# Optimization experiments

Measured on AMD Instinct MI355X. Metric: run time of the kernel, lower is better.

The kernel has to match this reference:

```python
import math
import jax, jax.numpy as jnp
import numpy as np

B, S, D, H, DFF, BASE = 2, 2048, 1024, 16, 4096, 10000.0
HD = D // H  # 64


def setup_inputs() -> dict:
    key = jax.random.key(0)
    ks = jax.random.split(key, 16)
    sc = 0.02
    inp = {
        "x": jax.random.normal(ks[0], (B, S, D), jnp.float32),
        "positions": jnp.arange(S, dtype=jnp.int32),
        "wq": jax.random.normal(ks[1], (D, D), jnp.float32) * sc,
        "bq": jnp.zeros((D,), jnp.float32),
        "wk": jax.random.normal(ks[2], (D, D), jnp.float32) * sc,
        "bk": jnp.zeros((D,), jnp.float32),
        "wv": jax.random.normal(ks[3], (D, D), jnp.float32) * sc,
        "bv": jnp.zeros((D,), jnp.float32),
        "wo": jax.random.normal(ks[4], (D, D), jnp.float32) * sc,
        "bo": jnp.zeros((D,), jnp.float32),
        "phase_bias": jax.random.uniform(ks[5], (H, HD), jnp.float32, -2.0 * math.pi, 0.0),
        "w1": jax.random.normal(ks[6], (D, DFF), jnp.float32) * sc,
        "b1": jnp.zeros((DFF,), jnp.float32),
        "w2": jax.random.normal(ks[7], (DFF, D), jnp.float32) * sc,
        "b2": jnp.zeros((D,), jnp.float32),
        "g1": jnp.ones((D,), jnp.float32),
        "be1": jnp.zeros((D,), jnp.float32),
        "g2": jnp.ones((D,), jnp.float32),
        "be2": jnp.zeros((D,), jnp.float32),
    }
    return inp


def _layernorm(x, g, b):
    mu = jnp.mean(x, -1, keepdims=True)
    var = jnp.mean(jnp.square(x - mu), -1, keepdims=True)
    return (x - mu) / jnp.sqrt(var + 1e-5) * g + b


def _block(x, positions, wq, bq, wk, bk, wv, bv, wo, bo, phase_bias,
           w1, b1, w2, b2, g1, be1, g2, be2):
    # projections -> (B, H, S, HD)
    def heads(w, b):
        return (x @ w + b).reshape(B, S, H, HD).transpose(0, 2, 1, 3)
    q, k, v = heads(wq, bq), heads(wk, bk), heads(wv, bv)

    # PoPE: magnitudes via softplus, phases from position*freq (+ clamped bias for k)
    mu_q = jax.nn.softplus(q)
    mu_k = jax.nn.softplus(k)
    freqs = 1.0 / BASE ** (jnp.arange(HD, dtype=jnp.float32) / HD)      # (HD,)
    pos_ph = positions[:, None].astype(jnp.float32) * freqs[None, :]     # (S, HD)
    q_ph = pos_ph[None, None]                                            # (1,1,S,HD)
    cb = jnp.clip(phase_bias, -2.0 * math.pi, 0.0)
    k_ph = pos_ph[None, None] + cb[None, :, None, :]                     # (1,H,S,HD)
    q_p = jnp.concatenate([mu_q * jnp.cos(q_ph), mu_q * jnp.sin(q_ph)], -1)  # (B,H,S,2HD)
    k_p = jnp.concatenate([mu_k * jnp.cos(k_ph), mu_k * jnp.sin(k_ph)], -1)

    # manual attention with causal mask and softmax1
    scale = 1.0 / math.sqrt(2 * HD)
    scores = jnp.einsum("bhqd,bhkd->bhqk", q_p, k_p) * scale
    causal = jnp.triu(jnp.ones((S, S), bool), 1)
    scores = jnp.where(causal, -jnp.inf, scores)
    m = jnp.max(scores, -1, keepdims=True)  # finite: diagonal always unmasked
    e = jnp.exp(scores - m)
    w = e / (jnp.exp(-m) + jnp.sum(e, -1, keepdims=True))
    attn = jnp.einsum("bhqk,bhkd->bhqd", w, v)
    attn = attn.transpose(0, 2, 1, 3).reshape(B, S, D) @ wo + bo

    h = _layernorm(x + attn, g1, be1)
    ff = jax.nn.relu(h @ w1 + b1) @ w2 + b2
    return _layernorm(h + ff, g2, be2)


def reference(x, positions, wq, bq, wk, bk, wv, bv, wo, bo, phase_bias,
              w1, b1, w2, b2, g1, be1, g2, be2):
    return _block(x, positions, wq, bq, wk, bk, wv, bv, wo, bo, phase_bias,
                  w1, b1, w2, b2, g1, be1, g2, be2)
```

## Files before the change

### kernel.cpp

```cpp
#include <hip/hip_runtime.h>
#include <hip/hip_bf16.h>
#include <math.h>

#define NB 2
#define NS 2048
#define ND 1024
#define NH 16
#define NHD 64
#define NDFF 4096

typedef __attribute__((ext_vector_type(4))) float f32x4;
typedef __attribute__((ext_vector_type(8))) short bf16x8;

__device__ __forceinline__ short f2bf(float f) {
  union { float f; unsigned u; } v; v.f = f;
  unsigned r = v.u + 0x7fffu + ((v.u >> 16) & 1u);
  return (short)(r >> 16);
}
__device__ __forceinline__ float bf2f(unsigned short u) {
  union { unsigned u; float f; } v; v.u = ((unsigned)u) << 16; return v.f;
}
__device__ __forceinline__ float softplus_f(float x) {
  return fmaxf(x, 0.f) + log1pf(__expf(-fabsf(x)));
}
__device__ __forceinline__ void gl16(const short* g, short* l) {
  __builtin_amdgcn_global_load_lds(
      (const __attribute__((address_space(1))) void*)g,
      (__attribute__((address_space(3))) void*)l, 16, 0, 0);
}
__device__ __forceinline__ void xcd_map(int& row0, int& col0) {
  const int gx = gridDim.x, gy = gridDim.y;
  const int bid = blockIdx.y * gx + blockIdx.x;
  const int rows_px = gy >> 3;
  const int xcd = bid & 7, l = bid >> 3;
  row0 = (xcd * rows_px + (l % rows_px)) * 128;
  col0 = (l / rows_px) * 128;
}

__global__ __launch_bounds__(256) void k_wt6(
    const float* __restrict__ wq, const float* __restrict__ wk,
    const float* __restrict__ wv, const float* __restrict__ wo,
    const float* __restrict__ w1, const float* __restrict__ w2,
    short* __restrict__ wqT, short* __restrict__ wkT, short* __restrict__ wvT,
    short* __restrict__ woT, short* __restrict__ w1T, short* __restrict__ w2T) {
  __shared__ float t[64][65];
  const int bid = blockIdx.x;
  const float* W; short* Wt; int K, N, local;
  if (bid < 1024) {
    const int wsel = bid >> 8; local = bid & 255;
    W  = wsel == 0 ? wq  : wsel == 1 ? wk  : wsel == 2 ? wv  : wo;
    Wt = wsel == 0 ? wqT : wsel == 1 ? wkT : wsel == 2 ? wvT : woT;
    K = ND; N = ND;
  } else if (bid < 2048) {
    local = bid - 1024; W = w1; Wt = w1T; K = ND; N = NDFF;
  } else {
    local = bid - 2048; W = w2; Wt = w2T; K = NDFF; N = ND;
  }
  const int nx = N >> 6;
  const int n0 = (local % nx) * 64, k0 = (local / nx) * 64;
  for (int i = threadIdx.x; i < 4096; i += 256) {
    const int r = i >> 6, c = i & 63;
    t[r][c] = W[(size_t)(k0 + r) * N + n0 + c];
  }
  __syncthreads();
  for (int i = threadIdx.x; i < 4096; i += 256) {
    const int r = i >> 6, c = i & 63;
    Wt[(size_t)(n0 + r) * K + k0 + c] = f2bf(t[c][r]);
  }
}

__global__ __launch_bounds__(256) void k_xb(const float* __restrict__ x,
    short* __restrict__ xb, int n8) {
  const int i = blockIdx.x * 256 + threadIdx.x;
  if (i >= n8) return;
  const float4 a = ((const float4*)x)[i * 2];
  const float4 b = ((const float4*)x)[i * 2 + 1];
  short tmp[8] = { f2bf(a.x), f2bf(a.y), f2bf(a.z), f2bf(a.w),
                   f2bf(b.x), f2bf(b.y), f2bf(b.z), f2bf(b.w) };
  *(int4*)&xb[(size_t)i * 8] = *(const int4*)tmp;
}

__global__ __launch_bounds__(256) void k_prep_v(const short* __restrict__ vb,
    short* __restrict__ vt) {
  __shared__ short t[64][72];
  const int bh = blockIdx.y, b = bh >> 4, h = bh & 15;
  const int s0 = blockIdx.x * 64;
  for (int i = threadIdx.x; i < 512; i += 256) {
    const int sl = i >> 3, d8 = (i & 7) * 8;
    int4 vv = *(const int4*)&vb[((size_t)(b * NS + s0 + sl) * NH + h) * NHD + d8];
    const short* sp = (const short*)&vv;
#pragma unroll
    for (int j = 0; j < 8; j++) t[d8 + j][sl] = sp[j];
  }
  __syncthreads();
  for (int i = threadIdx.x; i < 512; i += 256) {
    const int d = i >> 3, c8 = (i & 7) * 8;
    *(int4*)&vt[((size_t)bh * 64 + d) * NS + s0 + c8] = *(const int4*)&t[d][c8];
  }
}

__global__ __launch_bounds__(256) void k_pope(const short* __restrict__ qb,
    const short* __restrict__ kb, const int* __restrict__ positions,
    const float* __restrict__ phb, short* __restrict__ qp,
    short* __restrict__ kp) {
  const size_t i8 = ((size_t)blockIdx.x * 256 + threadIdx.x) * 8;
  const int d0 = (int)(i8 & 63);
  const int h  = (int)((i8 >> 6) & 15);
  const int s  = (int)((i8 >> 10) & 2047);
  const int b  = (int)(i8 >> 21);
  const float posf = (float)positions[s];
  int4 qv = *(const int4*)&qb[i8];
  int4 kv = *(const int4*)&kb[i8];
  const short* qs = (const short*)&qv;
  const short* ks = (const short*)&kv;
  short qc[8], qsn[8], kc[8], ksn[8];
#pragma unroll
  for (int j = 0; j < 8; j++) {
    const int d = d0 + j;
    const float freq = __expf(-(float)d * (float)(9.210340371976184 / 64.0));
    const float muq = softplus_f(bf2f((unsigned short)qs[j]));
    const float muk = softplus_f(bf2f((unsigned short)ks[j]));
    float cb = phb[h * 64 + d];
    cb = fminf(fmaxf(cb, -6.283185307179586f), 0.f);
    float snq, csq, snk, csk;
    __sincosf(posf * freq, &snq, &csq);
    __sincosf(posf * freq + cb, &snk, &csk);
    qc[j] = f2bf(muq * csq); qsn[j] = f2bf(muq * snq);
    kc[j] = f2bf(muk * csk); ksn[j] = f2bf(muk * snk);
  }
  const size_t o = (((size_t)(b * 16 + h) * NS + s) * 128) + d0;
  *(int4*)&qp[o] = *(const int4*)qc;
  *(int4*)&qp[o + 64] = *(const int4*)qsn;
  *(int4*)&kp[o] = *(const int4*)kc;
  *(int4*)&kp[o + 64] = *(const int4*)ksn;
}

#define BKK 32

__device__ __forceinline__ void gemm_core(const short* __restrict__ A,
    const short* __restrict__ Wt, const int K, const int kbeg, const int kend,
    const int row0, const int col0, short* lsA, short* lsB, f32x4 acc[4][4]) {
  const int tid = threadIdx.x;
  const int lane = tid & 63, wave = tid >> 6;
  const int lr = lane & 15, lk8 = (lane >> 4) << 3;
  const int wr = wave >> 1, wc = wave & 1;
  const int srow = lane >> 2, scol = (lane & 3) << 3;
  const int wbase = wave * 32;
#pragma unroll
  for (int m = 0; m < 4; m++)
#pragma unroll
    for (int n = 0; n < 4; n++) acc[m][n] = 0.f;
  const short* gA0 = &A[(size_t)(row0 + wbase + srow) * K + scol];
  const short* gA1 = gA0 + (size_t)16 * K;
  const short* gB0 = &Wt[(size_t)(col0 + wbase + srow) * K + scol];
  const short* gB1 = gB0 + (size_t)16 * K;
  short* const lA0 = lsA + wbase * 32;
  short* const lB0 = lsB + wbase * 32;
  auto stage = [&](int buf, int kk) {
    const int o = buf * 4096;
    gl16(gA0 + kk, lA0 + o);
    gl16(gA1 + kk, lA0 + o + 512);
    gl16(gB0 + kk, lB0 + o);
    gl16(gB1 + kk, lB0 + o + 512);
  };
  stage(0, kbeg);
  __syncthreads();
  int cur = 0;
  for (int k0 = kbeg; k0 < kend; k0 += BKK) {
    if (k0 + BKK < kend) stage(cur ^ 1, k0 + BKK);
    const short* la = lsA + cur * 4096;
    const short* lb = lsB + cur * 4096;
    bf16x8 af[4], bf_[4];
#pragma unroll
    for (int m = 0; m < 4; m++)
      af[m] = *(const bf16x8*)&la[(wr * 64 + m * 16 + lr) * 32 + lk8];
#pragma unroll
    for (int n = 0; n < 4; n++)
      bf_[n] = *(const bf16x8*)&lb[(wc * 64 + n * 16 + lr) * 32 + lk8];
#pragma unroll
    for (int m = 0; m < 4; m++)
#pragma unroll
      for (int n = 0; n < 4; n++)
        acc[m][n] = __builtin_amdgcn_mfma_f32_16x16x32_bf16(af[m], bf_[n], acc[m][n], 0, 0, 0);
    __syncthreads();
    cur ^= 1;
  }
}

template<int RELU, int OUTBF16>
__global__ __launch_bounds__(256) void k_gemm(const short* __restrict__ A,
    const short* __restrict__ Wt, const float* __restrict__ bias,
    void* __restrict__ C, int M, int N, int K) {
  __shared__ short lsA[2 * 4096], lsB[2 * 4096];
  f32x4 acc[4][4];
  int row0, col0;
  xcd_map(row0, col0);
  gemm_core(A, Wt, K, 0, K, row0, col0, lsA, lsB, acc);
  const int lane = threadIdx.x & 63, wave = threadIdx.x >> 6;
  const int lr = lane & 15, r4 = (lane >> 4) << 2;
  const int wr = wave >> 1, wc = wave & 1;
#pragma unroll
  for (int m = 0; m < 4; m++) {
#pragma unroll
    for (int n = 0; n < 4; n++) {
      const int col = col0 + wc * 64 + n * 16 + lr;
      const float bv = bias[col];
#pragma unroll
      for (int r = 0; r < 4; r++) {
        const int row = row0 + wr * 64 + m * 16 + r4 + r;
        float val = acc[m][n][r] + bv;
        if (RELU) val = fmaxf(val, 0.f);
        if (OUTBF16) ((short*)C)[(size_t)row * N + col] = f2bf(val);
        else ((float*)C)[(size_t)row * N + col] = val;
      }
    }
  }
}

__global__ __launch_bounds__(256) void k_gemm3(const short* __restrict__ xb,
    const short* __restrict__ wqT, const short* __restrict__ wkT,
    const short* __restrict__ wvT, const float* __restrict__ bq,
    const float* __restrict__ bk, const float* __restrict__ bv,
    short* __restrict__ qb, short* __restrict__ kb, short* __restrict__ vb) {
  __shared__ short lsA[2 * 4096], lsB[2 * 4096];
  const int z = blockIdx.z;
  const short* Wt = (z == 0) ? wqT : (z == 1) ? wkT : wvT;
  const float* bias = (z == 0) ? bq : (z == 1) ? bk : bv;
  short* C = (z == 0) ? qb : (z == 1) ? kb : vb;
  f32x4 acc[4][4];
  int row0, col0;
  xcd_map(row0, col0);
  gemm_core(xb, Wt, ND, 0, ND, row0, col0, lsA, lsB, acc);
  const int lane = threadIdx.x & 63, wave = threadIdx.x >> 6;
  const int lr = lane & 15, r4 = (lane >> 4) << 2;
  const int wr = wave >> 1, wc = wave & 1;
#pragma unroll
  for (int m = 0; m < 4; m++) {
#pragma unroll
    for (int n = 0; n < 4; n++) {
      const int col = col0 + wc * 64 + n * 16 + lr;
      const float bvs = bias[col];
#pragma unroll
      for (int r = 0; r < 4; r++) {
        const int row = row0 + wr * 64 + m * 16 + r4 + r;
        C[(size_t)row * ND + col] = f2bf(acc[m][n][r] + bvs);
      }
    }
  }
}

__global__ __launch_bounds__(256) void k_gemm_sk(const short* __restrict__ A,
    const short* __restrict__ Wt, float* __restrict__ C0, float* __restrict__ C1,
    int M, int N, int K) {
  __shared__ short lsA[2 * 4096], lsB[2 * 4096];
  f32x4 acc[4][4];
  const int z = blockIdx.z;
  const int khalf = K >> 1, kbeg = z * khalf, kend = kbeg + khalf;
  int row0, col0;
  xcd_map(row0, col0);
  gemm_core(A, Wt, K, kbeg, kend, row0, col0, lsA, lsB, acc);
  float* C = z ? C1 : C0;
  const int lane = threadIdx.x & 63, wave = threadIdx.x >> 6;
  const int lr = lane & 15, r4 = (lane >> 4) << 2;
  const int wr = wave >> 1, wc = wave & 1;
#pragma unroll
  for (int m = 0; m < 4; m++) {
#pragma unroll
    for (int n = 0; n < 4; n++) {
      const int col = col0 + wc * 64 + n * 16 + lr;
#pragma unroll
      for (int r = 0; r < 4; r++) {
        const int row = row0 + wr * 64 + m * 16 + r4 + r;
        C[(size_t)row * N + col] = acc[m][n][r];
      }
    }
  }
}

__device__ __forceinline__ void attn_proc(const bf16x8 aq[4], f32x4 acc_o[4],
    float l_p[4], const int rowb, const int kb,
    const short (*kpl)[136], const short (*vl)[72], short (*pl)[72],
    const int lr, const int lk) {
  f32x4 s_acc[4];
#pragma unroll
  for (int n = 0; n < 4; n++) s_acc[n] = 0.f;
#pragma unroll
  for (int ks = 0; ks < 4; ks++) {
    bf16x8 bk_[4];
#pragma unroll
    for (int n = 0; n < 4; n++)
      bk_[n] = *(const bf16x8*)&kpl[n * 16 + lr][ks * 32 + lk * 8];
#pragma unroll
    for (int n = 0; n < 4; n++)
      s_acc[n] = __builtin_amdgcn_mfma_f32_16x16x32_bf16(aq[ks], bk_[n], s_acc[n], 0, 0, 0);
  }
  const float scale = 0.08838834764831845f;
  const bool domask = (kb + 63 > rowb);
#pragma unroll
  for (int n = 0; n < 4; n++) {
#pragma unroll
    for (int r = 0; r < 4; r++) {
      const float sv = s_acc[n][r] * scale;
      float p;
      if (domask) {
        const int rel = rowb + lk * 4 + r - kb;
        p = (n * 16 + lr <= rel) ? __expf(sv) : 0.f;
      } else {
        p = __expf(sv);
      }
      s_acc[n][r] = p;
      l_p[r] += p;
    }
  }
#pragma unroll
  for (int n = 0; n < 4; n++)
#pragma unroll
    for (int r = 0; r < 4; r++)
      pl[lk * 4 + r][n * 16 + lr] = f2bf(s_acc[n][r]);
#pragma unroll
  for (int ks = 0; ks < 2; ks++) {
    const bf16x8 ap = *(const bf16x8*)&pl[lr][ks * 32 + lk * 8];
    bf16x8 bv_[4];
#pragma unroll
    for (int nd = 0; nd < 4; nd++)
      bv_[nd] = *(const bf16x8*)&vl[nd * 16 + lr][ks * 32 + lk * 8];
#pragma unroll
    for (int nd = 0; nd < 4; nd++)
      acc_o[nd] = __builtin_amdgcn_mfma_f32_16x16x32_bf16(ap, bv_[nd], acc_o[nd], 0, 0, 0);
  }
}

__global__ __launch_bounds__(512) void k_attn3(
    const short* __restrict__ qp, const short* __restrict__ kp,
    const short* __restrict__ vt, short* __restrict__ attn) {
  __shared__ short kp_l[2][64][136];
  __shared__ short v_l[2][64][72];
  __shared__ short p_l[8][16][72];
  const int bh = blockIdx.y, b = bh >> 4, h = bh & 15;
  const int bx = blockIdx.x;
  const int tid = threadIdx.x, wave = tid >> 6, lane = tid & 63;
  const int lr = lane & 15, lk = lane >> 4;
  const int tHeavy = 31 - bx;
  const int myTile = (wave < 4) ? tHeavy : bx;
  const int rowb = myTile * 64 + (wave & 3) * 16;
  const int nch = tHeavy + 1;

  bf16x8 aq[4];
  {
    const short* qrow = qp + ((size_t)bh * NS + rowb + lr) * 128;
#pragma unroll
    for (int ks = 0; ks < 4; ks++)
      aq[ks] = *(const bf16x8*)&qrow[ks * 32 + lk * 8];
  }
  f32x4 acc[4];
  float lsum[4];
#pragma unroll
  for (int r = 0; r < 4; r++) lsum[r] = 0.f;
#pragma unroll
  for (int n = 0; n < 4; n++) acc[n] = 0.f;

  const short* kpb = kp + (size_t)bh * NS * 128;
  const short* vtb = vt + (size_t)bh * 64 * NS;
  const int krow = tid >> 3, kcol = (tid & 7) * 16;
  const int vrow = tid >> 3, vcol = (tid & 7) * 8;

  int4 rk0, rk1, rv;
  {
    const short* s = &kpb[(size_t)krow * 128 + kcol];
    rk0 = ((const int4*)s)[0]; rk1 = ((const int4*)s)[1];
    rv = *(const int4*)&vtb[(size_t)vrow * NS + vcol];
  }
  ((int4*)&kp_l[0][krow][kcol])[0] = rk0;
  ((int4*)&kp_l[0][krow][kcol])[1] = rk1;
  *(int4*)&v_l[0][vrow][vcol] = rv;
  __syncthreads();

  for (int c = 0; c < nch; c++) {
    const int kb = c * 64;
    const int cur = c & 1;
    const bool more = (c + 1) < nch;
    if (more) {
      const int kb2 = kb + 64;
      const short* s = &kpb[(size_t)(kb2 + krow) * 128 + kcol];
      rk0 = ((const int4*)s)[0]; rk1 = ((const int4*)s)[1];
      rv = *(const int4*)&vtb[(size_t)vrow * NS + kb2 + vcol];
    }
    if (rowb + 15 >= kb)
      attn_proc(aq, acc, lsum, rowb, kb, kp_l[cur], v_l[cur], p_l[wave], lr, lk);
    if (more) {
      ((int4*)&kp_l[cur ^ 1][krow][kcol])[0] = rk0;
      ((int4*)&kp_l[cur ^ 1][krow][kcol])[1] = rk1;
      *(int4*)&v_l[cur ^ 1][vrow][vcol] = rv;
    }
    __syncthreads();
  }
#pragma unroll
  for (int r = 0; r < 4; r++) {
    float s = lsum[r];
#pragma unroll
    for (int off = 8; off; off >>= 1) s += __shfl_xor(s, off);
    lsum[r] = 1.f / (1.f + s);
  }
#pragma unroll
  for (int nd = 0; nd < 4; nd++) {
#pragma unroll
    for (int r = 0; r < 4; r++) {
      const int d = nd * 16 + lr;
      const int row = rowb + lk * 4 + r;
      attn[(((size_t)b * NS + row) * NH + h) * NHD + d] = f2bf(acc[nd][r] * lsum[r]);
    }
  }
}

template<int RBF16, int OUTBF16>
__global__ __launch_bounds__(256) void k_ln3(const float* __restrict__ A0,
    const float* __restrict__ A1, const float* __restrict__ badd,
    const void* __restrict__ Rv, const float* __restrict__ g,
    const float* __restrict__ be, void* __restrict__ out) {
  const int row = blockIdx.x, tid = threadIdx.x;
  const float4 a0 = ((const float4*)(A0 + (size_t)row * ND))[tid];
  const float4 a1 = ((const float4*)(A1 + (size_t)row * ND))[tid];
  const float4 bd = ((const float4*)badd)[tid];
  float r0, r1, r2, r3;
  if (RBF16) {
    short4 rr = *(const short4*)((const short*)Rv + (size_t)row * ND + tid * 4);
    r0 = bf2f((unsigned short)rr.x); r1 = bf2f((unsigned short)rr.y);
    r2 = bf2f((unsigned short)rr.z); r3 = bf2f((unsigned short)rr.w);
  } else {
    const float4 rr = ((const float4*)((const float*)Rv + (size_t)row * ND))[tid];
    r0 = rr.x; r1 = rr.y; r2 = rr.z; r3 = rr.w;
  }
  const float x0 = a0.x + a1.x + bd.x + r0;
  const float x1 = a0.y + a1.y + bd.y + r1;
  const float x2 = a0.z + a1.z + bd.z + r2;
  const float x3 = a0.w + a1.w + bd.w + r3;
  float s = x0 + x1 + x2 + x3;
  float sq = x0 * x0 + x1 * x1 + x2 * x2 + x3 * x3;
#pragma unroll
  for (int off = 32; off; off >>= 1) {
    s += __shfl_xor(s, off);
    sq += __shfl_xor(sq, off);
  }
  __shared__ float ss[4], ssq[4];
  const int wave = tid >> 6, lane = tid & 63;
  if (lane == 0) { ss[wave] = s; ssq[wave] = sq; }
  __syncthreads();
  s = ss[0] + ss[1] + ss[2] + ss[3];
  sq = ssq[0] + ssq[1] + ssq[2] + ssq[3];
  const float mu = s * (1.f / (float)ND);
  const float var = sq * (1.f / (float)ND) - mu * mu;
  const float rstd = rsqrtf(var + 1e-5f);
  const float4 gg = ((const float4*)g)[tid];
  const float4 bb = ((const float4*)be)[tid];
  const float o0 = (x0 - mu) * rstd * gg.x + bb.x;
  const float o1 = (x1 - mu) * rstd * gg.y + bb.y;
  const float o2 = (x2 - mu) * rstd * gg.z + bb.z;
  const float o3 = (x3 - mu) * rstd * gg.w + bb.w;
  if (OUTBF16) {
    short4 ov = { f2bf(o0), f2bf(o1), f2bf(o2), f2bf(o3) };
    *(short4*)((short*)out + (size_t)row * ND + tid * 4) = ov;
  } else {
    float4 ov = { o0, o1, o2, o3 };
    ((float4*)((float*)out + (size_t)row * ND))[tid] = ov;
  }
}

extern "C" void kernel_launch(void* const* d_in, const int* in_sizes, int n_in,
                              void* d_out, int out_size, void* d_ws, size_t ws_size,
                              hipStream_t stream) {
  const float* x   = (const float*)d_in[0];
  const int*   pos = (const int*)d_in[1];
  const float* wq  = (const float*)d_in[2];
  const float* bq  = (const float*)d_in[3];
  const float* wk  = (const float*)d_in[4];
  const float* bk  = (const float*)d_in[5];
  const float* wv  = (const float*)d_in[6];
  const float* bv  = (const float*)d_in[7];
  const float* wo  = (const float*)d_in[8];
  const float* bo  = (const float*)d_in[9];
  const float* phb = (const float*)d_in[10];
  const float* w1  = (const float*)d_in[11];
  const float* b1  = (const float*)d_in[12];
  const float* w2  = (const float*)d_in[13];
  const float* b2  = (const float*)d_in[14];
  const float* g1  = (const float*)d_in[15];
  const float* be1 = (const float*)d_in[16];
  const float* g2  = (const float*)d_in[17];
  const float* be2 = (const float*)d_in[18];

  char* ws = (char*)d_ws;
  const size_t MB = 1024 * 1024;
  if (ws_size < 112 * MB) return;
  short* qb     = (short*)(ws + 0 * MB);
  short* kb     = (short*)(ws + 8 * MB);
  short* vb     = (short*)(ws + 16 * MB);
  short* qp     = (short*)(ws + 24 * MB);
  short* kp     = (short*)(ws + 40 * MB);
  short* vt     = (short*)(ws + 56 * MB);
  short* xb     = (short*)(ws + 64 * MB);
  short* attnb  = (short*)(ws + 72 * MB);
  float* attnC0 = (float*)(ws + 0 * MB);
  float* attnC1 = (float*)(ws + 24 * MB);
  short* hb     = (short*)(ws + 16 * MB);
  short* ffh    = (short*)(ws + 40 * MB);
  float* ffC0   = (float*)(ws + 72 * MB);
  float* ffC1   = (float*)(ws + 0 * MB);
  short* wqT    = (short*)(ws + 88 * MB);
  short* wkT    = (short*)(ws + 90 * MB);
  short* wvT    = (short*)(ws + 92 * MB);
  short* woT    = (short*)(ws + 94 * MB);
  short* w1T    = (short*)(ws + 96 * MB);
  short* w2T    = (short*)(ws + 104 * MB);

  dim3 blk(256);
  k_wt6<<<dim3(3072), blk, 0, stream>>>(wq, wk, wv, wo, w1, w2,
                                        wqT, wkT, wvT, woT, w1T, w2T);
  k_xb<<<dim3((NB * NS * ND / 8 + 255) / 256), blk, 0, stream>>>(x, xb, NB * NS * ND / 8);
  k_gemm3<<<dim3(ND / 128, (NB * NS) / 128, 3), blk, 0, stream>>>(
      xb, wqT, wkT, wvT, bq, bk, bv, qb, kb, vb);
  k_pope<<<dim3(NB * NS * ND / 8 / 256), blk, 0, stream>>>(qb, kb, pos, phb, qp, kp);
  k_prep_v<<<dim3(NS / 64, NB * NH), blk, 0, stream>>>(vb, vt);
  k_attn3<<<dim3(16, NB * NH), dim3(512), 0, stream>>>(qp, kp, vt, attnb);
  k_gemm_sk<<<dim3(ND / 128, (NB * NS) / 128, 2), blk, 0, stream>>>(
      attnb, woT, attnC0, attnC1, NB * NS, ND, ND);
  k_ln3<0, 1><<<dim3(NB * NS), blk, 0, stream>>>(attnC0, attnC1, bo, x, g1, be1, hb);
  k_gemm<1, 1><<<dim3(NDFF / 128, (NB * NS) / 128), blk, 0, stream>>>(
      hb, w1T, b1, ffh, NB * NS, NDFF, ND);
  k_gemm_sk<<<dim3(ND / 128, (NB * NS) / 128, 2), blk, 0, stream>>>(
      ffh, w2T, ffC0, ffC1, NB * NS, ND, NDFF);
  k_ln3<1, 0><<<dim3(NB * NS), blk, 0, stream>>>(ffC0, ffC1, b2, hb, g2, be2, (float*)d_out);
}
```

Before: 278.6 us.

## Merge prep kernels and compute softmax row sums with MFMA against ones

```diff
diff --git a/kernel.cpp b/kernel.cpp
--- a/kernel.cpp
+++ b/kernel.cpp
@@ -37,14 +37,25 @@
   col0 = (l / rows_px) * 128;
 }
 
-__global__ __launch_bounds__(256) void k_wt6(
+__global__ __launch_bounds__(256) void k_prep(
     const float* __restrict__ wq, const float* __restrict__ wk,
     const float* __restrict__ wv, const float* __restrict__ wo,
     const float* __restrict__ w1, const float* __restrict__ w2,
+    const float* __restrict__ x,
     short* __restrict__ wqT, short* __restrict__ wkT, short* __restrict__ wvT,
-    short* __restrict__ woT, short* __restrict__ w1T, short* __restrict__ w2T) {
+    short* __restrict__ woT, short* __restrict__ w1T, short* __restrict__ w2T,
+    short* __restrict__ xb) {
   __shared__ float t[64][65];
   const int bid = blockIdx.x;
+  if (bid >= 3072) {
+    const int i = (bid - 3072) * 256 + threadIdx.x;
+    const float4 a = ((const float4*)x)[i * 2];
+    const float4 b = ((const float4*)x)[i * 2 + 1];
+    short tmp[8] = { f2bf(a.x), f2bf(a.y), f2bf(a.z), f2bf(a.w),
+                     f2bf(b.x), f2bf(b.y), f2bf(b.z), f2bf(b.w) };
+    *(int4*)&xb[(size_t)i * 8] = *(const int4*)tmp;
+    return;
+  }
   const float* W; short* Wt; int K, N, local;
   if (bid < 1024) {
     const int wsel = bid >> 8; local = bid & 255;
@@ -69,70 +80,60 @@
   }
 }
 
-__global__ __launch_bounds__(256) void k_xb(const float* __restrict__ x,
-    short* __restrict__ xb, int n8) {
-  const int i = blockIdx.x * 256 + threadIdx.x;
-  if (i >= n8) return;
-  const float4 a = ((const float4*)x)[i * 2];
-  const float4 b = ((const float4*)x)[i * 2 + 1];
-  short tmp[8] = { f2bf(a.x), f2bf(a.y), f2bf(a.z), f2bf(a.w),
-                   f2bf(b.x), f2bf(b.y), f2bf(b.z), f2bf(b.w) };
-  *(int4*)&xb[(size_t)i * 8] = *(const int4*)tmp;
-}
-
-__global__ __launch_bounds__(256) void k_prep_v(const short* __restrict__ vb,
-    short* __restrict__ vt) {
+__global__ __launch_bounds__(256) void k_pope_pv(const short* __restrict__ qb,
+    const short* __restrict__ kb, const short* __restrict__ vb,
+    const int* __restrict__ positions, const float* __restrict__ phb,
+    short* __restrict__ qp, short* __restrict__ kp, short* __restrict__ vt) {
   __shared__ short t[64][72];
-  const int bh = blockIdx.y, b = bh >> 4, h = bh & 15;
-  const int s0 = blockIdx.x * 64;
-  for (int i = threadIdx.x; i < 512; i += 256) {
-    const int sl = i >> 3, d8 = (i & 7) * 8;
-    int4 vv = *(const int4*)&vb[((size_t)(b * NS + s0 + sl) * NH + h) * NHD + d8];
-    const short* sp = (const short*)&vv;
-#pragma unroll
-    for (int j = 0; j < 8; j++) t[d8 + j][sl] = sp[j];
-  }
-  __syncthreads();
-  for (int i = threadIdx.x; i < 512; i += 256) {
-    const int d = i >> 3, c8 = (i & 7) * 8;
-    *(int4*)&vt[((size_t)bh * 64 + d) * NS + s0 + c8] = *(const int4*)&t[d][c8];
-  }
-}
-
-__global__ __launch_bounds__(256) void k_pope(const short* __restrict__ qb,
-    const short* __restrict__ kb, const int* __restrict__ positions,
-    const float* __restrict__ phb, short* __restrict__ qp,
-    short* __restrict__ kp) {
-  const size_t i8 = ((size_t)blockIdx.x * 256 + threadIdx.x) * 8;
-  const int d0 = (int)(i8 & 63);
-  const int h  = (int)((i8 >> 6) & 15);
-  const int s  = (int)((i8 >> 10) & 2047);
-  const int b  = (int)(i8 >> 21);
-  const float posf = (float)positions[s];
-  int4 qv = *(const int4*)&qb[i8];
-  int4 kv = *(const int4*)&kb[i8];
-  const short* qs = (const short*)&qv;
-  const short* ks = (const short*)&kv;
-  short qc[8], qsn[8], kc[8], ksn[8];
-#pragma unroll
-  for (int j = 0; j < 8; j++) {
-    const int d = d0 + j;
-    const float freq = __expf(-(float)d * (float)(9.210340371976184 / 64.0));
-    const float muq = softplus_f(bf2f((unsigned short)qs[j]));
-    const float muk = softplus_f(bf2f((unsigned short)ks[j]));
-    float cb = phb[h * 64 + d];
-    cb = fminf(fmaxf(cb, -6.283185307179586f), 0.f);
-    float snq, csq, snk, csk;
-    __sincosf(posf * freq, &snq, &csq);
-    __sincosf(posf * freq + cb, &snk, &csk);
-    qc[j] = f2bf(muq * csq); qsn[j] = f2bf(muq * snq);
-    kc[j] = f2bf(muk * csk); ksn[j] = f2bf(muk * snk);
-  }
-  const size_t o = (((size_t)(b * 16 + h) * NS + s) * 128) + d0;
-  *(int4*)&qp[o] = *(const int4*)qc;
-  *(int4*)&qp[o + 64] = *(const int4*)qsn;
-  *(int4*)&kp[o] = *(const int4*)kc;
-  *(int4*)&kp[o + 64] = *(const int4*)ksn;
+  const int bid = blockIdx.x;
+  if (bid < 2048) {
+    const size_t i8 = ((size_t)bid * 256 + threadIdx.x) * 8;
+    const int d0 = (int)(i8 & 63);
+    const int h  = (int)((i8 >> 6) & 15);
+    const int s  = (int)((i8 >> 10) & 2047);
+    const int b  = (int)(i8 >> 21);
+    const float posf = (float)positions[s];
+    int4 qv = *(const int4*)&qb[i8];
+    int4 kv = *(const int4*)&kb[i8];
+    const short* qs = (const short*)&qv;
+    const short* ks = (const short*)&kv;
+    short qc[8], qsn[8], kc[8], ksn[8];
+#pragma unroll
+    for (int j = 0; j < 8; j++) {
+      const int d = d0 + j;
+      const float freq = __expf(-(float)d * (float)(9.210340371976184 / 64.0));
+      const float muq = softplus_f(bf2f((unsigned short)qs[j]));
+      const float muk = softplus_f(bf2f((unsigned short)ks[j]));
+      float cb = phb[h * 64 + d];
+      cb = fminf(fmaxf(cb, -6.283185307179586f), 0.f);
+      float snq, csq, snk, csk;
+      __sincosf(posf * freq, &snq, &csq);
+      __sincosf(posf * freq + cb, &snk, &csk);
+      qc[j] = f2bf(muq * csq); qsn[j] = f2bf(muq * snq);
+      kc[j] = f2bf(muk * csk); ksn[j] = f2bf(muk * snk);
+    }
+    const size_t o = (((size_t)(b * 16 + h) * NS + s) * 128) + d0;
+    *(int4*)&qp[o] = *(const int4*)qc;
+    *(int4*)&qp[o + 64] = *(const int4*)qsn;
+    *(int4*)&kp[o] = *(const int4*)kc;
+    *(int4*)&kp[o + 64] = *(const int4*)ksn;
+  } else {
+    const int local = bid - 2048;
+    const int bh = local >> 5, b = bh >> 4, h = bh & 15;
+    const int s0 = (local & 31) * 64;
+    for (int i = threadIdx.x; i < 512; i += 256) {
+      const int sl = i >> 3, d8 = (i & 7) * 8;
+      int4 vv = *(const int4*)&vb[((size_t)(b * NS + s0 + sl) * NH + h) * NHD + d8];
+      const short* sp = (const short*)&vv;
+#pragma unroll
+      for (int j = 0; j < 8; j++) t[d8 + j][sl] = sp[j];
+    }
+    __syncthreads();
+    for (int i = threadIdx.x; i < 512; i += 256) {
+      const int d = i >> 3, c8 = (i & 7) * 8;
+      *(int4*)&vt[((size_t)bh * 64 + d) * NS + s0 + c8] = *(const int4*)&t[d][c8];
+    }
+  }
 }
 
 #define BKK 32
@@ -278,7 +279,7 @@
 }
 
 __device__ __forceinline__ void attn_proc(const bf16x8 aq[4], f32x4 acc_o[4],
-    float l_p[4], const int rowb, const int kb,
+    f32x4& accS, const int rowb, const int kb,
     const short (*kpl)[136], const short (*vl)[72], short (*pl)[72],
     const int lr, const int lk) {
   f32x4 s_acc[4];
@@ -294,22 +295,18 @@
     for (int n = 0; n < 4; n++)
       s_acc[n] = __builtin_amdgcn_mfma_f32_16x16x32_bf16(aq[ks], bk_[n], s_acc[n], 0, 0, 0);
   }
-  const float scale = 0.08838834764831845f;
+  const float scale2 = 0.1275174333f;
   const bool domask = (kb + 63 > rowb);
 #pragma unroll
   for (int n = 0; n < 4; n++) {
 #pragma unroll
     for (int r = 0; r < 4; r++) {
-      const float sv = s_acc[n][r] * scale;
-      float p;
+      float p = exp2f(s_acc[n][r] * scale2);
       if (domask) {
         const int rel = rowb + lk * 4 + r - kb;
-        p = (n * 16 + lr <= rel) ? __expf(sv) : 0.f;
-      } else {
-        p = __expf(sv);
+        p = (n * 16 + lr <= rel) ? p : 0.f;
       }
       s_acc[n][r] = p;
-      l_p[r] += p;
     }
   }
 #pragma unroll
@@ -317,9 +314,13 @@
 #pragma unroll
     for (int r = 0; r < 4; r++)
       pl[lk * 4 + r][n * 16 + lr] = f2bf(s_acc[n][r]);
+  bf16x8 bones;
+#pragma unroll
+  for (int i = 0; i < 8; i++) bones[i] = (short)0x3F80;
 #pragma unroll
   for (int ks = 0; ks < 2; ks++) {
     const bf16x8 ap = *(const bf16x8*)&pl[lr][ks * 32 + lk * 8];
+    accS = __builtin_amdgcn_mfma_f32_16x16x32_bf16(ap, bones, accS, 0, 0, 0);
     bf16x8 bv_[4];
 #pragma unroll
     for (int nd = 0; nd < 4; nd++)
@@ -352,10 +353,8 @@
     for (int ks = 0; ks < 4; ks++)
       aq[ks] = *(const bf16x8*)&qrow[ks * 32 + lk * 8];
   }
-  f32x4 acc[4];
-  float lsum[4];
-#pragma unroll
-  for (int r = 0; r < 4; r++) lsum[r] = 0.f;
+  f32x4 acc[4], accS;
+  accS = 0.f;
 #pragma unroll
   for (int n = 0; n < 4; n++) acc[n] = 0.f;
 
@@ -386,7 +385,7 @@
       rv = *(const int4*)&vtb[(size_t)vrow * NS + kb2 + vcol];
     }
     if (rowb + 15 >= kb)
-      attn_proc(aq, acc, lsum, rowb, kb, kp_l[cur], v_l[cur], p_l[wave], lr, lk);
+      attn_proc(aq, acc, accS, rowb, kb, kp_l[cur], v_l[cur], p_l[wave], lr, lk);
     if (more) {
       ((int4*)&kp_l[cur ^ 1][krow][kcol])[0] = rk0;
       ((int4*)&kp_l[cur ^ 1][krow][kcol])[1] = rk1;
@@ -394,20 +393,16 @@
     }
     __syncthreads();
   }
-#pragma unroll
-  for (int r = 0; r < 4; r++) {
-    float s = lsum[r];
-#pragma unroll
-    for (int off = 8; off; off >>= 1) s += __shfl_xor(s, off);
-    lsum[r] = 1.f / (1.f + s);
-  }
+  float inv[4];
+#pragma unroll
+  for (int r = 0; r < 4; r++) inv[r] = 1.f / (1.f + accS[r]);
 #pragma unroll
   for (int nd = 0; nd < 4; nd++) {
 #pragma unroll
     for (int r = 0; r < 4; r++) {
       const int d = nd * 16 + lr;
       const int row = rowb + lk * 4 + r;
-      attn[(((size_t)b * NS + row) * NH + h) * NHD + d] = f2bf(acc[nd][r] * lsum[r]);
+      attn[(((size_t)b * NS + row) * NH + h) * NHD + d] = f2bf(acc[nd][r] * inv[r]);
     }
   }
 }
@@ -513,13 +508,11 @@
   short* w2T    = (short*)(ws + 104 * MB);
 
   dim3 blk(256);
-  k_wt6<<<dim3(3072), blk, 0, stream>>>(wq, wk, wv, wo, w1, w2,
-                                        wqT, wkT, wvT, woT, w1T, w2T);
-  k_xb<<<dim3((NB * NS * ND / 8 + 255) / 256), blk, 0, stream>>>(x, xb, NB * NS * ND / 8);
+  k_prep<<<dim3(5120), blk, 0, stream>>>(wq, wk, wv, wo, w1, w2, x,
+                                         wqT, wkT, wvT, woT, w1T, w2T, xb);
   k_gemm3<<<dim3(ND / 128, (NB * NS) / 128, 3), blk, 0, stream>>>(
       xb, wqT, wkT, wvT, bq, bk, bv, qb, kb, vb);
-  k_pope<<<dim3(NB * NS * ND / 8 / 256), blk, 0, stream>>>(qb, kb, pos, phb, qp, kp);
-  k_prep_v<<<dim3(NS / 64, NB * NH), blk, 0, stream>>>(vb, vt);
+  k_pope_pv<<<dim3(3072), blk, 0, stream>>>(qb, kb, vb, pos, phb, qp, kp, vt);
   k_attn3<<<dim3(16, NB * NH), dim3(512), 0, stream>>>(qp, kp, vt, attnb);
   k_gemm_sk<<<dim3(ND / 128, (NB * NS) / 128, 2), blk, 0, stream>>>(
       attnb, woT, attnC0, attnC1, NB * NS, ND, ND);
```

Measured after the change: 275.6 us. About the same (-1.1%).
